# Performance work log

Measured on AMD Instinct MI355X. Metric: run time of the kernel, lower is better.

The kernel has to match this reference:

```python
import jax, jax.numpy as jnp
import numpy as np

D_K = 64

def setup_inputs() -> dict:
    key = jax.random.key(0)
    kq, kk, kv, km = jax.random.split(key, 4)
    B, H, S, D = 2, 16, 2048, D_K
    Q = jax.random.normal(kq, (B, H, S, D), dtype=jnp.float32)
    K = jax.random.normal(kk, (B, H, S, D), dtype=jnp.float32)
    V = jax.random.normal(kv, (B, H, S, D), dtype=jnp.float32)
    attn_mask = jax.random.bernoulli(km, 0.9, (B, H, S))  # True = valid
    return {"Q": Q, "K": K, "V": V, "attn_mask": attn_mask}

def reference(Q, K, V, attn_mask):
    # scores: [B, H, S, S]
    scores = jnp.einsum('bhqd,bhkd->bhqk', Q, K) / np.sqrt(D_K).astype(np.float32)
    fill = jnp.float32(1e-9)
    # mask rows (query positions) then columns (key positions), as in original
    scores = jnp.where(attn_mask[..., :, None], scores, fill)
    scores = jnp.where(attn_mask[..., None, :], scores, fill)
    attn = jax.nn.softmax(scores, axis=-1)
    context = jnp.einsum('bhqk,bhkd->bhqd', attn, V)
    return (context, attn)
```

## Files before the change

### kernel.cpp

```cpp
#include <hip/hip_runtime.h>

#define B_DIM 2
#define H_DIM 16
#define S_DIM 2048
#define D_DIM 64

constexpr int QB = 64;
constexpr int KB = 64;
constexpr int NT = S_DIM / KB;
constexpr float CL2E = 0.18033688011112042f;

typedef __attribute__((ext_vector_type(8))) short short8;
typedef __attribute__((ext_vector_type(4))) float f32x4;
typedef __attribute__((ext_vector_type(2))) unsigned uint2v;

__device__ __forceinline__ unsigned pkbf(float lo, float hi) {
  unsigned r;
  asm("v_cvt_pk_bf16_f32 %0, %1, %2" : "=v"(r) : "v"(lo), "v"(hi));
  return r;
}

__device__ __forceinline__ float fexp2(float x) {
  float r;
  asm("v_exp_f32 %0, %1" : "=v"(r) : "v"(x));
  return r;
}

__device__ __forceinline__ void barrier_lds() {
  asm volatile("s_waitcnt lgkmcnt(0)" ::: "memory");
  __builtin_amdgcn_s_barrier();
  asm volatile("" ::: "memory");
}

__global__ __launch_bounds__(256, 4)
void sdpa_kernel(const float* __restrict__ Qp, const float* __restrict__ Kp,
                 const float* __restrict__ Vp, const int* __restrict__ maskp,
                 float* __restrict__ ctx, float* __restrict__ attn)
{
  __shared__ __align__(16) unsigned short sK[2][KB * 64];
  __shared__ __align__(16) unsigned short sV[2][64 * KB];
  __shared__ __align__(16) unsigned short sP[4][16 * 64];

  const int tid  = threadIdx.x;
  const int wave = tid >> 6;
  const int lane = tid & 63;
  const int c = lane & 15;
  const int g = lane >> 4;

  const int bid = (blockIdx.x & 7) * 128 + (blockIdx.x >> 3);
  const int bh = bid >> 5;
  const int qt = bid & 31;
  const int q0 = qt * QB + wave * 16;
  const size_t bhS = (size_t)bh * S_DIM;

  const int key = tid >> 2;
  const int dq  = (tid & 3) << 4;
  const int kp  = (tid & 31) << 1;
  const int dq8 = (tid >> 5) << 3;

  short8 qf[2];
  #pragma unroll
  for (int kk = 0; kk < 2; ++kk) {
    const float* src = Qp + (bhS + (size_t)(q0 + c)) * D_DIM + kk*32 + g*8;
    float4 a = ((const float4*)src)[0];
    float4 b = ((const float4*)src)[1];
    union { unsigned u[4]; short8 s; } w;
    w.u[0] = pkbf(a.x, a.y); w.u[1] = pkbf(a.z, a.w);
    w.u[2] = pkbf(b.x, b.y); w.u[3] = pkbf(b.z, b.w);
    qf[kk] = w.s;
  }

  const float rvS = maskp[bhS + q0 + c] ? CL2E : 0.0f;

  float4 kr0, kr1, kr2, kr3;
  float4 vA0, vA1, vB0, vB1;
  unsigned kmr;

  auto load_k = [&](int kt_) {
    const float* s = Kp + (bhS + (size_t)(kt_ * KB + key)) * D_DIM + dq;
    kr0 = ((const float4*)s)[0]; kr1 = ((const float4*)s)[1];
    kr2 = ((const float4*)s)[2]; kr3 = ((const float4*)s)[3];
    kmr = maskp[bhS + kt_ * KB + key] ? 0xFFFFFFFFu : 0u;
  };
  auto load_v = [&](int kt_) {
    const float* s0 = Vp + (bhS + (size_t)(kt_ * KB + kp)) * D_DIM + dq8;
    vA0 = ((const float4*)s0)[0]; vA1 = ((const float4*)s0)[1];
    vB0 = ((const float4*)(s0 + D_DIM))[0]; vB1 = ((const float4*)(s0 + D_DIM))[1];
  };
  auto write_k = [&](int buf) {
    union { unsigned u[4]; short8 s; } w0, w1;
    w0.u[0] = pkbf(kr0.x, kr0.y) & kmr; w0.u[1] = pkbf(kr0.z, kr0.w) & kmr;
    w0.u[2] = pkbf(kr1.x, kr1.y) & kmr; w0.u[3] = pkbf(kr1.z, kr1.w) & kmr;
    w1.u[0] = pkbf(kr2.x, kr2.y) & kmr; w1.u[1] = pkbf(kr2.z, kr2.w) & kmr;
    w1.u[2] = pkbf(kr3.x, kr3.y) & kmr; w1.u[3] = pkbf(kr3.z, kr3.w) & kmr;
    const int sw = (key & 7) << 3;
    *(short8*)&sK[buf][key * 64 + (dq ^ sw)]       = w0.s;
    *(short8*)&sK[buf][key * 64 + ((dq + 8) ^ sw)] = w1.s;
  };
  auto write_v = [&](int buf) {
    float fa[8], fb[8];
    *(float4*)&fa[0] = vA0; *(float4*)&fa[4] = vA1;
    *(float4*)&fb[0] = vB0; *(float4*)&fb[4] = vB1;
    #pragma unroll
    for (int e = 0; e < 8; ++e) {
      const int d = dq8 + e;
      *(unsigned*)&sV[buf][d * KB + (kp ^ ((d & 7) << 3))] = pkbf(fa[e], fb[e]);
    }
  };

  float lsum = 0.0f;

  load_k(0);
  for (int kt = 0; kt < NT; ++kt) {
    const int cur = kt & 1;
    write_k(cur);
    if (kt + 1 < NT) load_k(kt + 1);
    barrier_lds();

    short8 kf[4][2];
    #pragma unroll
    for (int n = 0; n < 4; ++n) {
      const int k2 = n*16 + c;
      const int sw = (c & 7) << 3;
      #pragma unroll
      for (int kk = 0; kk < 2; ++kk)
        kf[n][kk] = *(const short8*)&sK[cur][k2*64 + ((kk*32 + g*8) ^ sw)];
    }

    f32x4 sacc[4];
    #pragma unroll
    for (int n = 0; n < 4; ++n) sacc[n] = 0.0f;
    __builtin_amdgcn_s_setprio(1);
    #pragma unroll
    for (int n = 0; n < 4; ++n)
      #pragma unroll
      for (int kk = 0; kk < 2; ++kk)
        sacc[n] = __builtin_amdgcn_mfma_f32_16x16x32_bf16(kf[n][kk], qf[kk], sacc[n], 0, 0, 0);
    __builtin_amdgcn_s_setprio(0);

    #pragma unroll
    for (int n = 0; n < 4; ++n)
      #pragma unroll
      for (int e = 0; e < 4; ++e)
        lsum += fexp2(sacc[n][e] * rvS);
  }

  float Lm;
  {
    float v = lsum;
    v += __shfl_xor(v, 16);
    v += __shfl_xor(v, 32);
    Lm = -__log2f(v);
  }

  f32x4 oacc[4];
  #pragma unroll
  for (int n = 0; n < 4; ++n) oacc[n] = 0.0f;

  unsigned short* const myP = sP[wave];
  const int rh  = lane >> 4;
  const int c16 = lane & 15;
  float* const abase = attn + (bhS + (size_t)q0) * S_DIM;

  auto copyout = [&](int kt_) {
    float* const at = abase + kt_*KB;
    #pragma unroll
    for (int j = 0; j < 4; ++j) {
      const int rr = j*4 + rh;
      const int p8 = (c16 >> 1) ^ (rr & 7);
      uint2v u = *(const uint2v*)&myP[rr*64 + p8*8 + (c16 & 1)*4];
      union { unsigned iu; float f; } t0, t1, t2, t3;
      t0.iu = u.x << 16; t1.iu = u.x & 0xFFFF0000u;
      t2.iu = u.y << 16; t3.iu = u.y & 0xFFFF0000u;
      f32x4 o; o[0] = t0.f; o[1] = t1.f; o[2] = t2.f; o[3] = t3.f;
      __builtin_nontemporal_store(o, (f32x4*)(at + (size_t)rr * S_DIM + c16*4));
    }
  };

  load_k(0); load_v(0);
  for (int kt = 0; kt < NT; ++kt) {
    const int cur = kt & 1;
    write_k(cur);
    write_v(cur);
    if (kt + 1 < NT) { load_k(kt + 1); load_v(kt + 1); }
    barrier_lds();

    short8 kf[4][2];
    #pragma unroll
    for (int n = 0; n < 4; ++n) {
      const int k2 = n*16 + c;
      const int sw = (c & 7) << 3;
      #pragma unroll
      for (int kk = 0; kk < 2; ++kk)
        kf[n][kk] = *(const short8*)&sK[cur][k2*64 + ((kk*32 + g*8) ^ sw)];
    }

    f32x4 sacc[4];
    #pragma unroll
    for (int n = 0; n < 4; ++n) sacc[n] = 0.0f;
    __builtin_amdgcn_s_setprio(1);
    #pragma unroll
    for (int n = 0; n < 4; ++n)
      #pragma unroll
      for (int kk = 0; kk < 2; ++kk)
        sacc[n] = __builtin_amdgcn_mfma_f32_16x16x32_bf16(kf[n][kk], qf[kk], sacc[n], 0, 0, 0);
    __builtin_amdgcn_s_setprio(0);

    #pragma unroll
    for (int n = 0; n < 4; ++n) {
      f32x4 pv;
      #pragma unroll
      for (int e = 0; e < 4; ++e)
        pv[e] = fexp2(__builtin_fmaf(sacc[n][e], rvS, Lm));
      const int swk = (n*16 + g*4) ^ ((c & 7) << 3);
      uint2v pr; pr.x = pkbf(pv[0], pv[1]); pr.y = pkbf(pv[2], pv[3]);
      *(uint2v*)&myP[c*64 + swk] = pr;
    }

    short8 pf[2];
    #pragma unroll
    for (int kk = 0; kk < 2; ++kk)
      pf[kk] = *(const short8*)&myP[c*64 + ((kk*32 + g*8) ^ ((c & 7) << 3))];
    __builtin_amdgcn_s_setprio(1);
    #pragma unroll
    for (int n = 0; n < 4; ++n) {
      const int d = n*16 + c;
      const int sw = (d & 7) << 3;
      #pragma unroll
      for (int kk = 0; kk < 2; ++kk) {
        short8 vf = *(const short8*)&sV[cur][d*KB + ((kk*32 + g*8) ^ sw)];
        oacc[n] = __builtin_amdgcn_mfma_f32_16x16x32_bf16(pf[kk], vf, oacc[n], 0, 0, 0);
      }
    }
    __builtin_amdgcn_s_setprio(0);

    copyout(kt);
  }

  #pragma unroll
  for (int n = 0; n < 4; ++n)
    #pragma unroll
    for (int e = 0; e < 4; ++e) {
      const int rl = g*4 + e;
      ctx[(bhS + (size_t)(q0 + rl)) * D_DIM + (size_t)(n*16 + c)] = oacc[n][e];
    }
}

extern "C" void kernel_launch(void* const* d_in, const int* in_sizes, int n_in,
                              void* d_out, int out_size, void* d_ws, size_t ws_size,
                              hipStream_t stream) {
  const float* Q = (const float*)d_in[0];
  const float* K = (const float*)d_in[1];
  const float* V = (const float*)d_in[2];
  const int*   M = (const int*)d_in[3];
  float* ctx  = (float*)d_out;
  float* attn = ctx + (size_t)B_DIM * H_DIM * S_DIM * D_DIM;
  dim3 grid(B_DIM * H_DIM * (S_DIM / QB));
  sdpa_kernel<<<grid, 256, 0, stream>>>(Q, K, V, M, ctx, attn);
}
```

Before: 161.7 us.

## Process two query tiles per block and fuse second tile's row-sum pass into first's output pass

Each block now runs 8 waves, and each wave handles two 16-row query tiles (X and Y), for 256 queries per block instead of 64. The first tile's output pass also computes the second tile's softmax normalizer, so K is streamed three times per two tiles instead of four. This cuts K/V global reads and bf16 conversion per query. In exchange the grid shrinks to 256 blocks of 512 threads and register pressure rises, which may hurt occupancy and load balance across CUs.

```diff
diff --git a/kernel.cpp b/kernel.cpp
--- a/kernel.cpp
+++ b/kernel.cpp
@@ -5,7 +5,6 @@
 #define S_DIM 2048
 #define D_DIM 64
 
-constexpr int QB = 64;
 constexpr int KB = 64;
 constexpr int NT = S_DIM / KB;
 constexpr float CL2E = 0.18033688011112042f;
@@ -32,14 +31,14 @@
   asm volatile("" ::: "memory");
 }
 
-__global__ __launch_bounds__(256, 4)
+__global__ __launch_bounds__(512, 2)
 void sdpa_kernel(const float* __restrict__ Qp, const float* __restrict__ Kp,
                  const float* __restrict__ Vp, const int* __restrict__ maskp,
                  float* __restrict__ ctx, float* __restrict__ attn)
 {
   __shared__ __align__(16) unsigned short sK[2][KB * 64];
   __shared__ __align__(16) unsigned short sV[2][64 * KB];
-  __shared__ __align__(16) unsigned short sP[4][16 * 64];
+  __shared__ __align__(16) unsigned short sP[8][16 * 64];
 
   const int tid  = threadIdx.x;
   const int wave = tid >> 6;
@@ -47,123 +46,77 @@
   const int c = lane & 15;
   const int g = lane >> 4;
 
-  const int bid = (blockIdx.x & 7) * 128 + (blockIdx.x >> 3);
-  const int bh = bid >> 5;
-  const int qt = bid & 31;
-  const int q0 = qt * QB + wave * 16;
+  const int bid = (blockIdx.x & 7) * 32 + (blockIdx.x >> 3);
+  const int bh = bid >> 3;
+  const int qt = bid & 7;
+  const int q0x = qt * 256 + wave * 16;
+  const int q0y = q0x + 128;
   const size_t bhS = (size_t)bh * S_DIM;
 
-  const int key = tid >> 2;
-  const int dq  = (tid & 3) << 4;
-  const int kp  = (tid & 31) << 1;
-  const int dq8 = (tid >> 5) << 3;
-
-  short8 qf[2];
+  const int keyk = tid >> 3;
+  const int dqk  = (tid & 7) << 3;
+  const int kpv  = (tid & 31) << 1;
+  const int d4   = (tid >> 5) << 2;
+
+  short8 qfX[2], qfY[2];
   #pragma unroll
   for (int kk = 0; kk < 2; ++kk) {
-    const float* src = Qp + (bhS + (size_t)(q0 + c)) * D_DIM + kk*32 + g*8;
-    float4 a = ((const float4*)src)[0];
-    float4 b = ((const float4*)src)[1];
+    const float* sx = Qp + (bhS + (size_t)(q0x + c)) * D_DIM + kk*32 + g*8;
+    float4 a = ((const float4*)sx)[0];
+    float4 b = ((const float4*)sx)[1];
     union { unsigned u[4]; short8 s; } w;
     w.u[0] = pkbf(a.x, a.y); w.u[1] = pkbf(a.z, a.w);
     w.u[2] = pkbf(b.x, b.y); w.u[3] = pkbf(b.z, b.w);
-    qf[kk] = w.s;
-  }
-
-  const float rvS = maskp[bhS + q0 + c] ? CL2E : 0.0f;
-
-  float4 kr0, kr1, kr2, kr3;
-  float4 vA0, vA1, vB0, vB1;
+    qfX[kk] = w.s;
+    const float* sy = Qp + (bhS + (size_t)(q0y + c)) * D_DIM + kk*32 + g*8;
+    float4 ay = ((const float4*)sy)[0];
+    float4 by = ((const float4*)sy)[1];
+    w.u[0] = pkbf(ay.x, ay.y); w.u[1] = pkbf(ay.z, ay.w);
+    w.u[2] = pkbf(by.x, by.y); w.u[3] = pkbf(by.z, by.w);
+    qfY[kk] = w.s;
+  }
+
+  const float rvSX = maskp[bhS + q0x + c] ? CL2E : 0.0f;
+  const float rvSY = maskp[bhS + q0y + c] ? CL2E : 0.0f;
+
+  float4 kA, kB;
+  float4 vA, vB;
   unsigned kmr;
 
   auto load_k = [&](int kt_) {
-    const float* s = Kp + (bhS + (size_t)(kt_ * KB + key)) * D_DIM + dq;
-    kr0 = ((const float4*)s)[0]; kr1 = ((const float4*)s)[1];
-    kr2 = ((const float4*)s)[2]; kr3 = ((const float4*)s)[3];
-    kmr = maskp[bhS + kt_ * KB + key] ? 0xFFFFFFFFu : 0u;
+    const float* s = Kp + (bhS + (size_t)(kt_ * KB + keyk)) * D_DIM + dqk;
+    kA = ((const float4*)s)[0]; kB = ((const float4*)s)[1];
+    kmr = maskp[bhS + kt_ * KB + keyk] ? 0xFFFFFFFFu : 0u;
   };
   auto load_v = [&](int kt_) {
-    const float* s0 = Vp + (bhS + (size_t)(kt_ * KB + kp)) * D_DIM + dq8;
-    vA0 = ((const float4*)s0)[0]; vA1 = ((const float4*)s0)[1];
-    vB0 = ((const float4*)(s0 + D_DIM))[0]; vB1 = ((const float4*)(s0 + D_DIM))[1];
+    const float* s0 = Vp + (bhS + (size_t)(kt_ * KB + kpv)) * D_DIM + d4;
+    vA = *(const float4*)s0;
+    vB = *(const float4*)(s0 + D_DIM);
   };
   auto write_k = [&](int buf) {
-    union { unsigned u[4]; short8 s; } w0, w1;
-    w0.u[0] = pkbf(kr0.x, kr0.y) & kmr; w0.u[1] = pkbf(kr0.z, kr0.w) & kmr;
-    w0.u[2] = pkbf(kr1.x, kr1.y) & kmr; w0.u[3] = pkbf(kr1.z, kr1.w) & kmr;
-    w1.u[0] = pkbf(kr2.x, kr2.y) & kmr; w1.u[1] = pkbf(kr2.z, kr2.w) & kmr;
-    w1.u[2] = pkbf(kr3.x, kr3.y) & kmr; w1.u[3] = pkbf(kr3.z, kr3.w) & kmr;
-    const int sw = (key & 7) << 3;
-    *(short8*)&sK[buf][key * 64 + (dq ^ sw)]       = w0.s;
-    *(short8*)&sK[buf][key * 64 + ((dq + 8) ^ sw)] = w1.s;
+    union { unsigned u[4]; short8 s; } w;
+    w.u[0] = pkbf(kA.x, kA.y) & kmr; w.u[1] = pkbf(kA.z, kA.w) & kmr;
+    w.u[2] = pkbf(kB.x, kB.y) & kmr; w.u[3] = pkbf(kB.z, kB.w) & kmr;
+    *(short8*)&sK[buf][keyk * 64 + (dqk ^ ((keyk & 7) << 3))] = w.s;
   };
   auto write_v = [&](int buf) {
-    float fa[8], fb[8];
-    *(float4*)&fa[0] = vA0; *(float4*)&fa[4] = vA1;
-    *(float4*)&fb[0] = vB0; *(float4*)&fb[4] = vB1;
-    #pragma unroll
-    for (int e = 0; e < 8; ++e) {
-      const int d = dq8 + e;
-      *(unsigned*)&sV[buf][d * KB + (kp ^ ((d & 7) << 3))] = pkbf(fa[e], fb[e]);
-    }
-  };
-
-  float lsum = 0.0f;
-
-  load_k(0);
-  for (int kt = 0; kt < NT; ++kt) {
-    const int cur = kt & 1;
-    write_k(cur);
-    if (kt + 1 < NT) load_k(kt + 1);
-    barrier_lds();
-
-    short8 kf[4][2];
-    #pragma unroll
-    for (int n = 0; n < 4; ++n) {
-      const int k2 = n*16 + c;
-      const int sw = (c & 7) << 3;
-      #pragma unroll
-      for (int kk = 0; kk < 2; ++kk)
-        kf[n][kk] = *(const short8*)&sK[cur][k2*64 + ((kk*32 + g*8) ^ sw)];
-    }
-
-    f32x4 sacc[4];
-    #pragma unroll
-    for (int n = 0; n < 4; ++n) sacc[n] = 0.0f;
-    __builtin_amdgcn_s_setprio(1);
-    #pragma unroll
-    for (int n = 0; n < 4; ++n)
-      #pragma unroll
-      for (int kk = 0; kk < 2; ++kk)
-        sacc[n] = __builtin_amdgcn_mfma_f32_16x16x32_bf16(kf[n][kk], qf[kk], sacc[n], 0, 0, 0);
-    __builtin_amdgcn_s_setprio(0);
-
-    #pragma unroll
-    for (int n = 0; n < 4; ++n)
-      #pragma unroll
-      for (int e = 0; e < 4; ++e)
-        lsum += fexp2(sacc[n][e] * rvS);
-  }
-
-  float Lm;
-  {
-    float v = lsum;
-    v += __shfl_xor(v, 16);
-    v += __shfl_xor(v, 32);
-    Lm = -__log2f(v);
-  }
-
-  f32x4 oacc[4];
-  #pragma unroll
-  for (int n = 0; n < 4; ++n) oacc[n] = 0.0f;
+    float fa[4], fb[4];
+    *(float4*)fa = vA; *(float4*)fb = vB;
+    #pragma unroll
+    for (int e = 0; e < 4; ++e) {
+      const int d = d4 + e;
+      *(unsigned*)&sV[buf][d * KB + (kpv ^ ((d & 7) << 3))] = pkbf(fa[e], fb[e]);
+    }
+  };
 
   unsigned short* const myP = sP[wave];
   const int rh  = lane >> 4;
   const int c16 = lane & 15;
-  float* const abase = attn + (bhS + (size_t)q0) * S_DIM;
-
-  auto copyout = [&](int kt_) {
-    float* const at = abase + kt_*KB;
+  float* const abx = attn + (bhS + (size_t)q0x) * S_DIM;
+  float* const aby = attn + (bhS + (size_t)q0y) * S_DIM;
+
+  auto copyout = [&](float* ab, int kt_) {
+    float* const at = ab + kt_*KB;
     #pragma unroll
     for (int j = 0; j < 4; ++j) {
       const int rr = j*4 + rh;
@@ -177,7 +130,136 @@
     }
   };
 
-  load_k(0); load_v(0);
+  auto read_kf = [&](int cur, short8 (&kf)[4][2]) {
+    #pragma unroll
+    for (int n = 0; n < 4; ++n) {
+      const int k2 = n*16 + c;
+      const int sw = (c & 7) << 3;
+      #pragma unroll
+      for (int kk = 0; kk < 2; ++kk)
+        kf[n][kk] = *(const short8*)&sK[cur][k2*64 + ((kk*32 + g*8) ^ sw)];
+    }
+  };
+
+  float lsumX = 0.0f;
+  load_k(0);
+  for (int kt = 0; kt < NT; ++kt) {
+    const int cur = kt & 1;
+    write_k(cur);
+    if (kt + 1 < NT) load_k(kt + 1);
+    else { load_k(0); load_v(0); }
+    barrier_lds();
+
+    short8 kf[4][2];
+    read_kf(cur, kf);
+    f32x4 sacc[4];
+    #pragma unroll
+    for (int n = 0; n < 4; ++n) sacc[n] = 0.0f;
+    __builtin_amdgcn_s_setprio(1);
+    #pragma unroll
+    for (int n = 0; n < 4; ++n)
+      #pragma unroll
+      for (int kk = 0; kk < 2; ++kk)
+        sacc[n] = __builtin_amdgcn_mfma_f32_16x16x32_bf16(kf[n][kk], qfX[kk], sacc[n], 0, 0, 0);
+    __builtin_amdgcn_s_setprio(0);
+    #pragma unroll
+    for (int n = 0; n < 4; ++n)
+      #pragma unroll
+      for (int e = 0; e < 4; ++e)
+        lsumX += fexp2(sacc[n][e] * rvSX);
+  }
+  float LmX;
+  {
+    float v = lsumX;
+    v += __shfl_xor(v, 16);
+    v += __shfl_xor(v, 32);
+    LmX = -__log2f(v);
+  }
+
+  f32x4 oaccX[4];
+  #pragma unroll
+  for (int n = 0; n < 4; ++n) oaccX[n] = 0.0f;
+  float lsumY = 0.0f;
+
+  for (int kt = 0; kt < NT; ++kt) {
+    const int cur = kt & 1;
+    write_k(cur);
+    write_v(cur);
+    if (kt + 1 < NT) { load_k(kt + 1); load_v(kt + 1); }
+    else { load_k(0); load_v(0); }
+    barrier_lds();
+
+    short8 kf[4][2];
+    read_kf(cur, kf);
+
+    f32x4 saccX[4], saccY[4];
+    #pragma unroll
+    for (int n = 0; n < 4; ++n) { saccX[n] = 0.0f; saccY[n] = 0.0f; }
+    __builtin_amdgcn_s_setprio(1);
+    #pragma unroll
+    for (int n = 0; n < 4; ++n)
+      #pragma unroll
+      for (int kk = 0; kk < 2; ++kk) {
+        saccX[n] = __builtin_amdgcn_mfma_f32_16x16x32_bf16(kf[n][kk], qfX[kk], saccX[n], 0, 0, 0);
+        saccY[n] = __builtin_amdgcn_mfma_f32_16x16x32_bf16(kf[n][kk], qfY[kk], saccY[n], 0, 0, 0);
+      }
+    __builtin_amdgcn_s_setprio(0);
+
+    #pragma unroll
+    for (int n = 0; n < 4; ++n) {
+      f32x4 pv;
+      #pragma unroll
+      for (int e = 0; e < 4; ++e)
+        pv[e] = fexp2(__builtin_fmaf(saccX[n][e], rvSX, LmX));
+      const int swk = (n*16 + g*4) ^ ((c & 7) << 3);
+      uint2v pr; pr.x = pkbf(pv[0], pv[1]); pr.y = pkbf(pv[2], pv[3]);
+      *(uint2v*)&myP[c*64 + swk] = pr;
+    }
+
+    #pragma unroll
+    for (int n = 0; n < 4; ++n)
+      #pragma unroll
+      for (int e = 0; e < 4; ++e)
+        lsumY += fexp2(saccY[n][e] * rvSY);
+
+    short8 pf[2];
+    #pragma unroll
+    for (int kk = 0; kk < 2; ++kk)
+      pf[kk] = *(const short8*)&myP[c*64 + ((kk*32 + g*8) ^ ((c & 7) << 3))];
+    __builtin_amdgcn_s_setprio(1);
+    #pragma unroll
+    for (int n = 0; n < 4; ++n) {
+      const int d = n*16 + c;
+      const int sw = (d & 7) << 3;
+      #pragma unroll
+      for (int kk = 0; kk < 2; ++kk) {
+        short8 vf = *(const short8*)&sV[cur][d*KB + ((kk*32 + g*8) ^ sw)];
+        oaccX[n] = __builtin_amdgcn_mfma_f32_16x16x32_bf16(pf[kk], vf, oaccX[n], 0, 0, 0);
+      }
+    }
+    __builtin_amdgcn_s_setprio(0);
+
+    copyout(abx, kt);
+  }
+
+  #pragma unroll
+  for (int n = 0; n < 4; ++n)
+    #pragma unroll
+    for (int e = 0; e < 4; ++e)
+      ctx[(bhS + (size_t)(q0x + g*4 + e)) * D_DIM + (size_t)(n*16 + c)] = oaccX[n][e];
+
+  float LmY;
+  {
+    float v = lsumY;
+    v += __shfl_xor(v, 16);
+    v += __shfl_xor(v, 32);
+    LmY = -__log2f(v);
+  }
+
+  f32x4 oaccY[4];
+  #pragma unroll
+  for (int n = 0; n < 4; ++n) oaccY[n] = 0.0f;
+
   for (int kt = 0; kt < NT; ++kt) {
     const int cur = kt & 1;
     write_k(cur);
@@ -186,24 +268,16 @@
     barrier_lds();
 
     short8 kf[4][2];
-    #pragma unroll
-    for (int n = 0; n < 4; ++n) {
-      const int k2 = n*16 + c;
-      const int sw = (c & 7) << 3;
+    read_kf(cur, kf);
+    f32x4 sacc[4];
+    #pragma unroll
+    for (int n = 0; n < 4; ++n) sacc[n] = 0.0f;
+    __builtin_amdgcn_s_setprio(1);
+    #pragma unroll
+    for (int n = 0; n < 4; ++n)
       #pragma unroll
       for (int kk = 0; kk < 2; ++kk)
-        kf[n][kk] = *(const short8*)&sK[cur][k2*64 + ((kk*32 + g*8) ^ sw)];
-    }
-
-    f32x4 sacc[4];
-    #pragma unroll
-    for (int n = 0; n < 4; ++n) sacc[n] = 0.0f;
-    __builtin_amdgcn_s_setprio(1);
-    #pragma unroll
-    for (int n = 0; n < 4; ++n)
-      #pragma unroll
-      for (int kk = 0; kk < 2; ++kk)
-        sacc[n] = __builtin_amdgcn_mfma_f32_16x16x32_bf16(kf[n][kk], qf[kk], sacc[n], 0, 0, 0);
+        sacc[n] = __builtin_amdgcn_mfma_f32_16x16x32_bf16(kf[n][kk], qfY[kk], sacc[n], 0, 0, 0);
     __builtin_amdgcn_s_setprio(0);
 
     #pragma unroll
@@ -211,7 +285,7 @@
       f32x4 pv;
       #pragma unroll
       for (int e = 0; e < 4; ++e)
-        pv[e] = fexp2(__builtin_fmaf(sacc[n][e], rvS, Lm));
+        pv[e] = fexp2(__builtin_fmaf(sacc[n][e], rvSY, LmY));
       const int swk = (n*16 + g*4) ^ ((c & 7) << 3);
       uint2v pr; pr.x = pkbf(pv[0], pv[1]); pr.y = pkbf(pv[2], pv[3]);
       *(uint2v*)&myP[c*64 + swk] = pr;
@@ -229,21 +303,19 @@
       #pragma unroll
       for (int kk = 0; kk < 2; ++kk) {
         short8 vf = *(const short8*)&sV[cur][d*KB + ((kk*32 + g*8) ^ sw)];
-        oacc[n] = __builtin_amdgcn_mfma_f32_16x16x32_bf16(pf[kk], vf, oacc[n], 0, 0, 0);
+        oaccY[n] = __builtin_amdgcn_mfma_f32_16x16x32_bf16(pf[kk], vf, oaccY[n], 0, 0, 0);
       }
     }
     __builtin_amdgcn_s_setprio(0);
 
-    copyout(kt);
+    copyout(aby, kt);
   }
 
   #pragma unroll
   for (int n = 0; n < 4; ++n)
     #pragma unroll
-    for (int e = 0; e < 4; ++e) {
-      const int rl = g*4 + e;
-      ctx[(bhS + (size_t)(q0 + rl)) * D_DIM + (size_t)(n*16 + c)] = oacc[n][e];
-    }
+    for (int e = 0; e < 4; ++e)
+      ctx[(bhS + (size_t)(q0y + g*4 + e)) * D_DIM + (size_t)(n*16 + c)] = oaccY[n][e];
 }
 
 extern "C" void kernel_launch(void* const* d_in, const int* in_sizes, int n_in,
@@ -255,6 +327,6 @@
   const int*   M = (const int*)d_in[3];
   float* ctx  = (float*)d_out;
   float* attn = ctx + (size_t)B_DIM * H_DIM * S_DIM * D_DIM;
-  dim3 grid(B_DIM * H_DIM * (S_DIM / QB));
-  sdpa_kernel<<<grid, 256, 0, stream>>>(Q, K, V, M, ctx, attn);
-}
+  dim3 grid(B_DIM * H_DIM * (S_DIM / 256));
+  sdpa_kernel<<<grid, 512, 0, stream>>>(Q, K, V, M, ctx, attn);
+}
```

Result: faster. 145.8 us (-9.9%).
